# Kernel tuning notes

Measured on AMD Instinct MI355X. Metric: run time of the kernel, lower is better.

Reference implementation:

```python
import jax, jax.numpy as jnp
import numpy as np

WIN = 1024
HOP = 256

def setup_inputs() -> dict:
    key = jax.random.key(0)
    x = jax.random.normal(key, (16, WIN, 2048), dtype=jnp.float32)
    return {"x": x}

def reference(x) -> jnp.ndarray:
    # Overlap-add: y[b, f*hop + c] += x[b, c, f]
    B, win, n_frames = x.shape
    hop = HOP
    out_len = (n_frames - 1) * hop + win
    idx = jnp.arange(win)[:, None] + hop * jnp.arange(n_frames)[None, :]
    y = jnp.zeros((B, out_len), dtype=x.dtype)
    y = y.at[:, idx].add(x)
    return y
```

## Files before the change

### kernel.cpp

```cpp
#include <hip/hip_runtime.h>


constexpr int BATCH   = 16;
constexpr int WIN     = 1024;
constexpr int HOP     = 256;
constexpr int NF      = 2048;
constexpr int OUT_LEN = (NF - 1) * HOP + WIN;
constexpr int GTOT    = OUT_LEN / HOP;
constexpr int FT      = 128;
constexpr int RBW     = 4;
constexpr int NBLK    = 512;

typedef float f4a __attribute__((ext_vector_type(4), aligned(16)));

__global__ __launch_bounds__(256, 2)
void oadd_kernel(const float* __restrict__ x, float* __restrict__ y) {
    __shared__ float L[4][2][4][RBW][FT];

    const int tid = threadIdx.x;
    const int w   = tid >> 6;
    const int l   = tid & 63;

    const int wid = blockIdx.x * 4 + w;
    const int b   = wid >> 7;
    const int rsp = (wid >> 1) & 63;
    const int tg  = wid & 1;
    const int T   = tg ? 9 : 8;
    const int rbase = rsp * RBW;

    const float* __restrict__ xb = x + (size_t)b * WIN * NF;
    float* __restrict__ yb = y + (size_t)b * OUT_LEN;

    const int ch = (l & 31) * 4;
    const int rh = l >> 5;

    auto fill = [&](int t, int s) {
        const int tile = tg * 8 + t;
        const bool m2  = (tile == 16);
        const int g0   = tile * FT;
        #pragma unroll
        for (int k = 0; k < 4; ++k) {
            const int col = m2 ? (NF - FT) + ch : g0 + ch - k;
            #pragma unroll
            for (int i = 0; i < 2; ++i) {
                const int row = k * HOP + rbase + i * 2 + rh;
                const float* src = xb + (size_t)row * NF + col;
                __builtin_amdgcn_global_load_lds(
                    (const __attribute__((address_space(1))) unsigned int*)src,
                    (__attribute__((address_space(3))) unsigned int*)&L[w][s][k][i * 2][0],
                    16, 0, 0);
            }
        }
    };

    auto phase2 = [&](int t, int s) {
        const int tile = tg * 8 + t;
        const int g0   = tile * FT;
        if (tile == 0) {
            #pragma unroll
            for (int p = 0; p < 2; ++p) {
                const int j = p * 64 + l;
                f4a v;
                #pragma unroll
                for (int m = 0; m < 4; ++m) {
                    float a = L[w][s][0][m][j];
                    if (j >= 1) a += L[w][s][1][m][j];
                    if (j >= 2) a += L[w][s][2][m][j];
                    if (j >= 3) a += L[w][s][3][m][j];
                    v[m] = a;
                }
                *reinterpret_cast<f4a*>(&yb[(size_t)(g0 + j) * HOP + rbase]) = v;
            }
        } else if (tile == 16) {
            if (l < 3) {
                const int j = l;
                f4a v;
                #pragma unroll
                for (int m = 0; m < 4; ++m) {
                    float a = 0.f;
                    #pragma unroll
                    for (int k = 1; k < 4; ++k)
                        if (k > j) a += L[w][s][k][m][FT - k + j];
                    v[m] = a;
                }
                *reinterpret_cast<f4a*>(&yb[(size_t)(g0 + j) * HOP + rbase]) = v;
            }
        } else {
            #pragma unroll
            for (int p = 0; p < 2; ++p) {
                const int j = p * 64 + l;
                f4a v;
                #pragma unroll
                for (int m = 0; m < 4; ++m) {
                    v[m] = (L[w][s][0][m][j] + L[w][s][1][m][j])
                         + (L[w][s][2][m][j] + L[w][s][3][m][j]);
                }
                *reinterpret_cast<f4a*>(&yb[(size_t)(g0 + j) * HOP + rbase]) = v;
            }
        }
    };

    fill(0, 0);
    for (int t = 0; t < T; ++t) {
        if (t + 1 < T) fill(t + 1, (t + 1) & 1);
        if (t == 0)         asm volatile("s_waitcnt vmcnt(8)"  ::: "memory");
        else if (t + 1 < T) asm volatile("s_waitcnt vmcnt(10)" ::: "memory");
        else                asm volatile("s_waitcnt vmcnt(2)"  ::: "memory");
        phase2(t, t & 1);
    }
}

extern "C" void kernel_launch(void* const* d_in, const int* in_sizes, int n_in,
                              void* d_out, int out_size, void* d_ws, size_t ws_size,
                              hipStream_t stream) {
    const float* x = (const float*)d_in[0];
    float* y = (float*)d_out;
    oadd_kernel<<<dim3(NBLK), 256, 0, stream>>>(x, y);
}
```

Baseline: 41.54 us.

## Deepen LDS prefetch pipeline and remap blocks to 16-row, 64-frame tiles

Each block now owns 16 output rows of one batch across half the frame tiles, instead of each wave owning 4 rows. Frame tiles shrink from 128 to 64, and the shared buffer becomes a 4-slot ring with prefetch depth 3, so more global-to-LDS loads are in flight while earlier tiles are summed. Output stores from the four waves now form 64-byte contiguous chunks. The cost is shorter contiguous read segments per row and more loop iterations per block.

```diff
diff --git a/kernel.cpp b/kernel.cpp
--- a/kernel.cpp
+++ b/kernel.cpp
@@ -7,106 +7,100 @@
 constexpr int NF      = 2048;
 constexpr int OUT_LEN = (NF - 1) * HOP + WIN;
 constexpr int GTOT    = OUT_LEN / HOP;
-constexpr int FT      = 128;
-constexpr int RBW     = 4;
+constexpr int FT      = 64;
+constexpr int NT      = (GTOT + FT - 1) / FT;
+constexpr int RB      = 16;
+constexpr int NBUF    = 4;
+constexpr int DEPTH   = 3;
 constexpr int NBLK    = 512;
 
 typedef float f4a __attribute__((ext_vector_type(4), aligned(16)));
 
 __global__ __launch_bounds__(256, 2)
 void oadd_kernel(const float* __restrict__ x, float* __restrict__ y) {
-    __shared__ float L[4][2][4][RBW][FT];
+    __shared__ float L[NBUF][4][RB][FT];
 
-    const int tid = threadIdx.x;
-    const int w   = tid >> 6;
-    const int l   = tid & 63;
-
-    const int wid = blockIdx.x * 4 + w;
-    const int b   = wid >> 7;
-    const int rsp = (wid >> 1) & 63;
-    const int tg  = wid & 1;
-    const int T   = tg ? 9 : 8;
-    const int rbase = rsp * RBW;
+    const int tid  = threadIdx.x;
+    const int w    = tid >> 6;
+    const int l    = tid & 63;
+    const int bid  = blockIdx.x;
+    const int half = bid >> 8;
+    const int b    = (bid >> 4) & 15;
+    const int rsp  = bid & 15;
+    const int rbase = rsp * RB;
+    const int tile0 = half ? 17 : 0;
+    const int T     = half ? 16 : 17;
 
     const float* __restrict__ xb = x + (size_t)b * WIN * NF;
     float* __restrict__ yb = y + (size_t)b * OUT_LEN;
 
-    const int ch = (l & 31) * 4;
-    const int rh = l >> 5;
+    const int sr = l >> 4;
+    const int c  = l & 15;
 
     auto fill = [&](int t, int s) {
-        const int tile = tg * 8 + t;
-        const bool m2  = (tile == 16);
+        const int tile = tile0 + t;
         const int g0   = tile * FT;
         #pragma unroll
         for (int k = 0; k < 4; ++k) {
-            const int col = m2 ? (NF - FT) + ch : g0 + ch - k;
-            #pragma unroll
-            for (int i = 0; i < 2; ++i) {
-                const int row = k * HOP + rbase + i * 2 + rh;
-                const float* src = xb + (size_t)row * NF + col;
-                __builtin_amdgcn_global_load_lds(
-                    (const __attribute__((address_space(1))) unsigned int*)src,
-                    (__attribute__((address_space(3))) unsigned int*)&L[w][s][k][i * 2][0],
-                    16, 0, 0);
-            }
+            const int col0 = (tile == NT - 1) ? (NF - FT) : (g0 - k);
+            const float* src = xb + (size_t)(k * HOP + rbase + w * 4 + sr) * NF
+                                  + col0 + c * 4;
+            __builtin_amdgcn_global_load_lds(
+                (const __attribute__((address_space(1))) unsigned int*)src,
+                (__attribute__((address_space(3))) unsigned int*)&L[s][k][w * 4][0],
+                16, 0, 0);
         }
     };
 
     auto phase2 = [&](int t, int s) {
-        const int tile = tg * 8 + t;
+        const int tile = tile0 + t;
         const int g0   = tile * FT;
         if (tile == 0) {
+            f4a v;
             #pragma unroll
-            for (int p = 0; p < 2; ++p) {
-                const int j = p * 64 + l;
+            for (int m = 0; m < 4; ++m) {
+                const int rl = w * 4 + m;
+                float a = L[s][0][rl][l];
+                if (l >= 1) a += L[s][1][rl][l];
+                if (l >= 2) a += L[s][2][rl][l];
+                if (l >= 3) a += L[s][3][rl][l];
+                v[m] = a;
+            }
+            *reinterpret_cast<f4a*>(&yb[(size_t)(g0 + l) * HOP + rbase + w * 4]) = v;
+        } else if (tile == NT - 1) {
+            if (l < 3) {
                 f4a v;
                 #pragma unroll
                 for (int m = 0; m < 4; ++m) {
-                    float a = L[w][s][0][m][j];
-                    if (j >= 1) a += L[w][s][1][m][j];
-                    if (j >= 2) a += L[w][s][2][m][j];
-                    if (j >= 3) a += L[w][s][3][m][j];
-                    v[m] = a;
-                }
-                *reinterpret_cast<f4a*>(&yb[(size_t)(g0 + j) * HOP + rbase]) = v;
-            }
-        } else if (tile == 16) {
-            if (l < 3) {
-                const int j = l;
-                f4a v;
-                #pragma unroll
-                for (int m = 0; m < 4; ++m) {
+                    const int rl = w * 4 + m;
                     float a = 0.f;
                     #pragma unroll
                     for (int k = 1; k < 4; ++k)
-                        if (k > j) a += L[w][s][k][m][FT - k + j];
+                        if (k > l) a += L[s][k][rl][FT - k + l];
                     v[m] = a;
                 }
-                *reinterpret_cast<f4a*>(&yb[(size_t)(g0 + j) * HOP + rbase]) = v;
+                *reinterpret_cast<f4a*>(&yb[(size_t)(g0 + l) * HOP + rbase + w * 4]) = v;
             }
         } else {
+            f4a v;
             #pragma unroll
-            for (int p = 0; p < 2; ++p) {
-                const int j = p * 64 + l;
-                f4a v;
-                #pragma unroll
-                for (int m = 0; m < 4; ++m) {
-                    v[m] = (L[w][s][0][m][j] + L[w][s][1][m][j])
-                         + (L[w][s][2][m][j] + L[w][s][3][m][j]);
-                }
-                *reinterpret_cast<f4a*>(&yb[(size_t)(g0 + j) * HOP + rbase]) = v;
+            for (int m = 0; m < 4; ++m) {
+                const int rl = w * 4 + m;
+                v[m] = (L[s][0][rl][l] + L[s][1][rl][l])
+                     + (L[s][2][rl][l] + L[s][3][rl][l]);
             }
+            *reinterpret_cast<f4a*>(&yb[(size_t)(g0 + l) * HOP + rbase + w * 4]) = v;
         }
     };
 
-    fill(0, 0);
+    fill(0, 0); fill(1, 1); fill(2, 2);
     for (int t = 0; t < T; ++t) {
-        if (t + 1 < T) fill(t + 1, (t + 1) & 1);
-        if (t == 0)         asm volatile("s_waitcnt vmcnt(8)"  ::: "memory");
-        else if (t + 1 < T) asm volatile("s_waitcnt vmcnt(10)" ::: "memory");
-        else                asm volatile("s_waitcnt vmcnt(2)"  ::: "memory");
-        phase2(t, t & 1);
+        if (t + DEPTH < T) fill(t + DEPTH, (t + DEPTH) & 3);
+        if (t + DEPTH < T)  asm volatile("s_waitcnt vmcnt(12)" ::: "memory");
+        else if (t + 2 < T) asm volatile("s_waitcnt vmcnt(8)"  ::: "memory");
+        else if (t + 1 < T) asm volatile("s_waitcnt vmcnt(4)"  ::: "memory");
+        else                asm volatile("s_waitcnt vmcnt(0)"  ::: "memory");
+        phase2(t, t & 3);
     }
 }
 
```

Result: faster. 36.15 us (-13.0%).
